# Kernel optimization log

Measured on AMD Instinct MI355X. Metric: run time of the kernel, lower is better.

Reference implementation:

```python
import jax, jax.numpy as jnp
import numpy as np

B, T, D = 4, 2048, 1024
H, KVH = 16, 4          # query heads, kv heads
HD = D // H             # head_dim = 64
R = 32                  # partial rope dims
ROPE_BASE = 10000.0
EPS = 1e-6


def rmsnorm(x, scale):
    # per-head RMSNorm over last dim, computed in fp32 like the torch code
    xf = x.astype(jnp.float32)
    norm = jax.lax.rsqrt(jnp.mean(xf * xf, axis=-1, keepdims=True) + EPS)
    return (xf * norm).astype(x.dtype) * scale


def apply_rope(x, cos, sin):
    # x: (B,T,H,HD); rotate first R dims, pass the rest through
    x_r, x_p = x[..., :R], x[..., R:]
    half = R // 2
    x1, x2 = x_r[..., :half], x_r[..., half:]
    rotated = jnp.concatenate([x1 * cos - x2 * sin, x1 * sin + x2 * cos], axis=-1)
    return jnp.concatenate([rotated, x_p], axis=-1)


def setup_inputs() -> dict:
    key = jax.random.key(0)
    ks = jax.random.split(key, 8)
    x = jax.random.normal(ks[0], (B, T, D), dtype=jnp.float32)
    # RoPE tables exactly as RotaryEmbedding.get_cos_sin
    inv_freq = 1.0 / (ROPE_BASE ** (jnp.arange(0, R, 2, dtype=jnp.float32) / R))
    t = jnp.arange(T, dtype=jnp.float32)
    freqs = jnp.outer(t, inv_freq)                      # (T, R/2)
    cos = jnp.cos(freqs)[None, :, None, :]              # (1,T,1,R/2)
    sin = jnp.sin(freqs)[None, :, None, :]
    s = 1.0 / np.sqrt(D)
    Wq = jax.random.normal(ks[1], (D, D), dtype=jnp.float32) * s
    Wk = jax.random.normal(ks[2], (KVH * HD, D), dtype=jnp.float32) * s
    Wv = jax.random.normal(ks[3], (KVH * HD, D), dtype=jnp.float32) * s
    Wo = jax.random.normal(ks[4], (D, D), dtype=jnp.float32) * s
    q_scale = jnp.ones((HD,), dtype=jnp.float32)
    k_scale = jnp.ones((HD,), dtype=jnp.float32)
    return {"x": x, "cos": cos, "sin": sin, "Wq": Wq, "Wk": Wk, "Wv": Wv,
            "Wo": Wo, "q_scale": q_scale, "k_scale": k_scale}


def reference(x, cos, sin, Wq, Wk, Wv, Wo, q_scale, k_scale):
    b, t, d = x.shape
    q = jnp.einsum('btd,ed->bte', x, Wq).reshape(b, t, H, HD)
    k = jnp.einsum('btd,ed->bte', x, Wk).reshape(b, t, KVH, HD)
    v = jnp.einsum('btd,ed->bte', x, Wv).reshape(b, t, KVH, HD)
    q = apply_rope(rmsnorm(q, q_scale), cos, sin)
    k = apply_rope(rmsnorm(k, k_scale), cos, sin)
    groups = H // KVH
    k = jnp.repeat(k, groups, axis=2)   # (b,t,H,HD), matches repeat_interleave dim=2
    v = jnp.repeat(v, groups, axis=2)
    q = q.transpose(0, 2, 1, 3)         # (b,H,t,HD)
    k = k.transpose(0, 2, 1, 3)
    v = v.transpose(0, 2, 1, 3)
    scores = jnp.einsum('bhqd,bhkd->bhqk', q, k) / np.sqrt(HD)
    causal = jnp.tril(jnp.ones((t, t), dtype=bool))
    scores = jnp.where(causal, scores, -jnp.inf)
    attn = jax.nn.softmax(scores, axis=-1)
    y = jnp.einsum('bhqk,bhkd->bhqd', attn, v)
    y = y.transpose(0, 2, 1, 3).reshape(b, t, d)
    return jnp.einsum('btd,ed->bte', y, Wo)
```

## Files before the change

kernel.cpp:

```cpp
#include <hip/hip_runtime.h>
#include <hip/hip_bf16.h>
#include <stdint.h>

typedef __attribute__((ext_vector_type(8)))  __bf16 bf16x8;
typedef __attribute__((ext_vector_type(4)))  float  f32x4;
typedef __attribute__((ext_vector_type(16))) float  f32x16;
typedef __hip_bfloat16 bf16_t;

#define T_SEQ 2048
#define D_MODEL 1024
#define N_HEADS 16
#define N_KV 4
#define HD 64
#define LDQKV 1536
#define KDIM 1024

__device__ inline void cvt16(const float4* __restrict__ g, int4* __restrict__ s) {
  float4 v0 = g[0], v1 = g[1], v2 = g[2], v3 = g[3];
  union { int4 i[2]; __hip_bfloat162 h[8]; } u;
  u.h[0] = __float22bfloat162_rn(make_float2(v0.x, v0.y));
  u.h[1] = __float22bfloat162_rn(make_float2(v0.z, v0.w));
  u.h[2] = __float22bfloat162_rn(make_float2(v1.x, v1.y));
  u.h[3] = __float22bfloat162_rn(make_float2(v1.z, v1.w));
  u.h[4] = __float22bfloat162_rn(make_float2(v2.x, v2.y));
  u.h[5] = __float22bfloat162_rn(make_float2(v2.z, v2.w));
  u.h[6] = __float22bfloat162_rn(make_float2(v3.x, v3.y));
  u.h[7] = __float22bfloat162_rn(make_float2(v3.z, v3.w));
  s[0] = u.i[0]; s[1] = u.i[1];
}

__device__ inline void storeC(bf16_t* p, float v) { *p = __float2bfloat16(v); }
__device__ inline void storeC(float* p, float v) { *p = v; }

__device__ inline void plswap(unsigned& a, unsigned& b) {
  asm volatile("v_permlane32_swap_b32 %0, %1" : "+v"(a), "+v"(b));
}

__device__ inline float fexp2(float x) {
  float r; asm("v_exp_f32 %0, %1" : "=v"(r) : "v"(x)); return r;
}
__device__ inline unsigned cvtpk(float lo, float hi) {
  unsigned r; asm("v_cvt_pk_bf16_f32 %0, %1, %2" : "=v"(r) : "v"(lo), "v"(hi));
  return r;
}

__device__ inline void gll16(const bf16_t* g, bf16_t* l) {
  __builtin_amdgcn_global_load_lds(
      (const __attribute__((address_space(1))) void*)g,
      (__attribute__((address_space(3))) void*)l, 16, 0, 0);
}

__global__ __launch_bounds__(256) void all_cvt(
    const float* __restrict__ x,
    const float* __restrict__ Wq, const float* __restrict__ Wk,
    const float* __restrict__ Wv, const float* __restrict__ Wo,
    bf16_t* __restrict__ xb, bf16_t* __restrict__ wqkvb,
    bf16_t* __restrict__ wob) {
  const int i = blockIdx.x * 256 + threadIdx.x;
  const float* s; bf16_t* d; int off;
  if (i < 524288)      { s = x;  d = xb;                   off = i; }
  else if (i < 589824) { s = Wq; d = wqkvb;                off = i - 524288; }
  else if (i < 606208) { s = Wk; d = wqkvb + 1024 * 1024;  off = i - 589824; }
  else if (i < 622592) { s = Wv; d = wqkvb + 1280 * 1024;  off = i - 606208; }
  else                 { s = Wo; d = wob;                  off = i - 622592; }
  cvt16((const float4*)s + off * 4, (int4*)d + off * 2);
}

template <int MODE, typename CT>
__global__ __launch_bounds__(256) void gemm_bb(
    const bf16_t* __restrict__ A, const bf16_t* __restrict__ W,
    CT* __restrict__ C, const int ldC,
    const float* __restrict__ cosb, const float* __restrict__ sinb,
    const float* __restrict__ qs, const float* __restrict__ ks,
    bf16_t* __restrict__ v_t)
{
  __shared__ bf16_t As[128 * 32];
  __shared__ bf16_t Bs[128 * 32];
  const int tid = threadIdx.x;
  const int lane = tid & 63;
  const int wv = tid >> 6;
  const int wr = wv >> 1, wc = wv & 1;
  const int m0 = blockIdx.y * 128;
  const int n0 = blockIdx.x * 128;

  const int srow = lane >> 2;
  const int scol = (lane & 3) * 8;
  const bf16_t* gA = A + (size_t)(m0 + 32 * wv + srow) * KDIM + scol;
  const bf16_t* gB = W + (size_t)(n0 + 32 * wv + srow) * KDIM + scol;
  bf16_t* lA = As + wv * 1024;
  bf16_t* lB = Bs + wv * 1024;

  f32x4 acc[4][4];
#pragma unroll
  for (int m = 0; m < 4; ++m)
#pragma unroll
    for (int n = 0; n < 4; ++n)
      acc[m][n] = {0.f, 0.f, 0.f, 0.f};

  const int fr = lane & 15;
  const int fq = lane >> 4;

  for (int k0 = 0; k0 < KDIM; k0 += 32) {
    gll16(gA + k0, lA);
    gll16(gA + 16 * KDIM + k0, lA + 512);
    gll16(gB + k0, lB);
    gll16(gB + 16 * KDIM + k0, lB + 512);
    __syncthreads();
    bf16x8 af[4], bfv[4];
#pragma unroll
    for (int m = 0; m < 4; ++m)
      af[m] = *(const bf16x8*)(&As[(wr * 64 + m * 16 + fr) * 32 + fq * 8]);
#pragma unroll
    for (int n = 0; n < 4; ++n)
      bfv[n] = *(const bf16x8*)(&Bs[(wc * 64 + n * 16 + fr) * 32 + fq * 8]);
#pragma unroll
    for (int m = 0; m < 4; ++m)
#pragma unroll
      for (int n = 0; n < 4; ++n)
        acc[m][n] = __builtin_amdgcn_mfma_f32_16x16x32_bf16(af[m], bfv[n],
                                                            acc[m][n], 0, 0, 0);
    __syncthreads();
  }

  if (MODE == 0 || n0 < 1280) {
    if (MODE == 1) {
      const float* stab = (n0 < 1024) ? qs : ks;
      float sc0 = stab[fr], sc1 = stab[16 + fr], sc2 = stab[32 + fr], sc3 = stab[48 + fr];
#pragma unroll
      for (int m = 0; m < 4; ++m)
#pragma unroll
        for (int r = 0; r < 4; ++r) {
          const int row = m0 + wr * 64 + m * 16 + fq * 4 + r;
          const int t = row & (T_SEQ - 1);
          float ss = acc[m][0][r] * acc[m][0][r] + acc[m][1][r] * acc[m][1][r]
                   + acc[m][2][r] * acc[m][2][r] + acc[m][3][r] * acc[m][3][r];
          ss += __shfl_xor(ss, 1);
          ss += __shfl_xor(ss, 2);
          ss += __shfl_xor(ss, 4);
          ss += __shfl_xor(ss, 8);
          const float nrm = rsqrtf(ss * (1.f / 64.f) + 1e-6f);
          const float v0 = acc[m][0][r] * nrm * sc0;
          const float v1 = acc[m][1][r] * nrm * sc1;
          const float v2 = acc[m][2][r] * nrm * sc2;
          const float v3 = acc[m][3][r] * nrm * sc3;
          const float c = cosb[t * 16 + fr];
          const float s = sinb[t * 16 + fr];
          const float r0 = v0 * c - v1 * s;
          const float r1 = v0 * s + v1 * c;
          bf16_t* p = (bf16_t*)C + (size_t)row * ldC + n0 + wc * 64 + fr;
          p[0]  = __float2bfloat16(r0);
          p[16] = __float2bfloat16(r1);
          p[32] = __float2bfloat16(v2);
          p[48] = __float2bfloat16(v3);
        }
    } else {
#pragma unroll
      for (int m = 0; m < 4; ++m)
#pragma unroll
        for (int n = 0; n < 4; ++n)
#pragma unroll
          for (int r = 0; r < 4; ++r) {
            const int row = wr * 64 + m * 16 + fq * 4 + r;
            const int col = wc * 64 + n * 16 + fr;
            storeC(&C[(size_t)(m0 + row) * ldC + n0 + col], acc[m][n][r]);
          }
    }
  } else {
#pragma unroll
    for (int m = 0; m < 4; ++m) {
      const int row0 = m0 + wr * 64 + m * 16 + fq * 4;
      const int b = row0 >> 11, t0 = row0 & (T_SEQ - 1);
#pragma unroll
      for (int n = 0; n < 4; ++n) {
        const int vcol = n0 - 1280 + wc * 64 + n * 16 + fr;
        const int g = b * 4 + (vcol >> 6);
        const int d = vcol & 63;
        uint2 pk2;
        pk2.x = cvtpk(acc[m][n][0], acc[m][n][1]);
        pk2.y = cvtpk(acc[m][n][2], acc[m][n][3]);
        *(uint2*)(v_t + ((size_t)g * HD + d) * T_SEQ + t0) = pk2;
      }
    }
  }
}

__global__ __launch_bounds__(512) void attn(
    const bf16_t* __restrict__ qkv, const bf16_t* __restrict__ v_t,
    bf16_t* __restrict__ y)
{
  __shared__ int4 lds[2048];
  const int tid  = threadIdx.x;
  const int lane = tid & 63;
  const int w    = tid >> 6;
  const int spair= w >> 1;
  const int h    = w & 1;
  const int ql   = lane & 31;
  const int hi   = lane >> 5;
  const int id   = (int)blockIdx.x;
  const int low3 = id & 7;
  const int rest = id >> 3;
  const int gsel = rest & 1;
  const int hh   = (rest >> 1) & 3;
  const int sbi  = rest >> 3;
  const int sb   = ((sbi >> 2) & 1) ? (sbi + 4 - ((sbi >> 3) << 4)) : (15 - sbi);
  const int g16  = low3 + 8 * gsel;
  const int b    = g16 >> 2, kvh = g16 & 3;
  const int hd   = kvh * 4 + hh;
  const int s    = 4 * sb + spair;
  const int q_glob = s * 32 + ql;
  const int nt   = s + 1;
  const int nR   = 2 * sb + 2;
  const float SCALE_LOG2 = 0.125f * 1.44269504089f;

  const int sid = tid & 255;
  const int u   = tid >> 8;
  const int kr = sid >> 3, kslot = sid & 7;
  const int vd = sid >> 2, vslot = sid & 3;
  const bf16_t* gK = qkv + (size_t)(b * T_SEQ + kr + u * 32) * LDQKV + 1024 + kvh * HD + kslot * 8;
  const bf16_t* gV = v_t + (size_t)((b * N_KV + kvh) * HD + vd) * T_SEQ + vslot * 8 + u * 32;
  const int wKidx = u * 256 + kr * 8 + (kslot ^ (kr & 7));
  const int wVidx = 512 + u * 256 + vd * 4 + (vslot ^ ((vd >> 1) & 3));

  int kridx[4];
#pragma unroll
  for (int c = 0; c < 4; ++c)
    kridx[c] = ql * 8 + ((2 * c + hi) ^ (ql & 7));
  const int vsw = (ql >> 1) & 3;
  const int v0idx = 512 + ql * 4 + (hi ^ vsw);
  const int v1idx = 512 + ql * 4 + ((2 + hi) ^ vsw);
  const int v2idx = 512 + (ql + 32) * 4 + (hi ^ vsw);
  const int v3idx = 512 + (ql + 32) * 4 + ((2 + hi) ^ vsw);

  union ob { unsigned uu[4]; bf16x8 v; } onesf;
#pragma unroll
  for (int i = 0; i < 4; ++i) onesf.uu[i] = 0x3F803F80u;

  f32x16 zro;
#pragma unroll
  for (int i = 0; i < 16; ++i) zro[i] = 0.f;

  float* lf = (float*)lds;

  const bf16_t* Qrow = qkv + (size_t)(b * T_SEQ + q_glob) * LDQKV + hd * HD + hi * 8;
  bf16x8 qfrag[4];
#pragma unroll
  for (int c = 0; c < 4; ++c) {
    bf16x8 raw = *(const bf16x8*)(Qrow + c * 16);
    bf16x8 sc;
#pragma unroll
    for (int j = 0; j < 8; ++j)
      sc[j] = (__bf16)((float)raw[j] * SCALE_LOG2);
    qfrag[c] = sc;
  }

  f32x16 acc0, acc1, accL;
#pragma unroll
  for (int i = 0; i < 16; ++i) { acc0[i] = 0.f; acc1[i] = 0.f; accL[i] = 0.f; }
  float m_run = -1e30f;

  {
    int4 kA = *(const int4*)gK;
    int4 vA = *(const int4*)gV;
    lds[wKidx] = kA;
    lds[wVidx] = vA;
  }
  __syncthreads();

  int buf = 0;
  for (int r = 0; r < nR; ++r) {
    int4 kA, vA;
    const bool more = (r + 1 < nR);
    if (more) {
      kA = *(const int4*)(gK + (size_t)(r + 1) * 64 * LDQKV);
      vA = *(const int4*)(gV + (r + 1) * 64);
    }

    const int t = 2 * r + h;
    if (t < nt) {
      const int k0 = t << 5;
      const bool masked = (t == nt - 1);
      const int base = buf * 1024 + h * 256;

      bf16x8 kf0 = *(const bf16x8*)&lds[base + kridx[0]];
      bf16x8 kf1 = *(const bf16x8*)&lds[base + kridx[1]];
      bf16x8 kf2 = *(const bf16x8*)&lds[base + kridx[2]];
      bf16x8 kf3 = *(const bf16x8*)&lds[base + kridx[3]];

      __builtin_amdgcn_s_setprio(1);
      f32x16 st = __builtin_amdgcn_mfma_f32_32x32x16_bf16(kf0, qfrag[0], zro, 0, 0, 0);
      st = __builtin_amdgcn_mfma_f32_32x32x16_bf16(kf1, qfrag[1], st, 0, 0, 0);
      st = __builtin_amdgcn_mfma_f32_32x32x16_bf16(kf2, qfrag[2], st, 0, 0, 0);
      st = __builtin_amdgcn_mfma_f32_32x32x16_bf16(kf3, qfrag[3], st, 0, 0, 0);
      __builtin_amdgcn_s_setprio(0);

      if (masked) {
#pragma unroll
        for (int rr = 0; rr < 16; ++rr) {
          const int kg = k0 + (rr & 3) + 8 * (rr >> 2) + 4 * hi;
          if (kg > q_glob) st[rr] = -1e30f;
        }
      }
      float m01 = fmaxf(fmaxf(st[0], st[1]), st[2]);
      float m02 = fmaxf(fmaxf(st[3], st[4]), st[5]);
      float m03 = fmaxf(fmaxf(st[6], st[7]), st[8]);
      float m04 = fmaxf(fmaxf(st[9], st[10]), st[11]);
      float m05 = fmaxf(fmaxf(st[12], st[13]), st[14]);
      float m06 = fmaxf(fmaxf(m01, m02), m03);
      float m07 = fmaxf(fmaxf(m04, m05), st[15]);
      const float bmax = fmaxf(m06, m07);
      if (__any(bmax > m_run + 8.f)) {
        const float rmax = fmaxf(bmax, __shfl_xor(bmax, 32));
        const float mnew = fmaxf(m_run, rmax);
        const float corr = fexp2(m_run - mnew);
#pragma unroll
        for (int i = 0; i < 16; ++i) { acc0[i] *= corr; acc1[i] *= corr; }
        accL[0] *= corr;
        m_run = mnew;
      }
      float pp[16];
#pragma unroll
      for (int rr = 0; rr < 16; ++rr) pp[rr] = fexp2(st[rr] - m_run);

      unsigned wp[8];
#pragma unroll
      for (int i = 0; i < 8; ++i) wp[i] = cvtpk(pp[2 * i], pp[2 * i + 1]);
      plswap(wp[0], wp[2]); plswap(wp[1], wp[3]);
      plswap(wp[4], wp[6]); plswap(wp[5], wp[7]);
      union fu { unsigned uu2[4]; bf16x8 v; };
      fu f1, f2;
      f1.uu2[0] = wp[0]; f1.uu2[1] = wp[1]; f1.uu2[2] = wp[2]; f1.uu2[3] = wp[3];
      f2.uu2[0] = wp[4]; f2.uu2[1] = wp[5]; f2.uu2[2] = wp[6]; f2.uu2[3] = wp[7];

      bf16x8 vf0 = *(const bf16x8*)&lds[base + v0idx];
      bf16x8 vf1 = *(const bf16x8*)&lds[base + v1idx];
      bf16x8 vf2 = *(const bf16x8*)&lds[base + v2idx];
      bf16x8 vf3 = *(const bf16x8*)&lds[base + v3idx];

      __builtin_amdgcn_s_setprio(1);
      acc0 = __builtin_amdgcn_mfma_f32_32x32x16_bf16(vf0, f1.v, acc0, 0, 0, 0);
      acc0 = __builtin_amdgcn_mfma_f32_32x32x16_bf16(vf1, f2.v, acc0, 0, 0, 0);
      acc1 = __builtin_amdgcn_mfma_f32_32x32x16_bf16(vf2, f1.v, acc1, 0, 0, 0);
      acc1 = __builtin_amdgcn_mfma_f32_32x32x16_bf16(vf3, f2.v, acc1, 0, 0, 0);
      accL = __builtin_amdgcn_mfma_f32_32x32x16_bf16(onesf.v, f1.v, accL, 0, 0, 0);
      accL = __builtin_amdgcn_mfma_f32_32x32x16_bf16(onesf.v, f2.v, accL, 0, 0, 0);
      __builtin_amdgcn_s_setprio(0);
    }

    if (more) {
      const int nb = (buf ^ 1) * 1024;
      lds[nb + wKidx] = kA;
      lds[nb + wVidx] = vA;
    }
    __syncthreads();
    buf ^= 1;
  }

  float cA = 1.f, cB = 0.f, l_mrg = 0.f;
  if (h == 1) {
    const int fb = spair * 1216 + lane * 19;
#pragma unroll
    for (int i = 0; i < 16; ++i) lf[fb + i] = acc0[i];
    lf[fb + 16] = m_run;
    lf[fb + 17] = accL[0];
  }
  __syncthreads();
  if (h == 0) {
    const int fb = spair * 1216 + lane * 19;
    const float mB = lf[fb + 16], lB = lf[fb + 17];
    const float mM = fmaxf(m_run, mB);
    cA = fexp2(m_run - mM);
    cB = fexp2(mB - mM);
    l_mrg = accL[0] * cA + lB * cB;
#pragma unroll
    for (int i = 0; i < 16; ++i) acc0[i] = acc0[i] * cA + lf[fb + i] * cB;
  }
  __syncthreads();
  if (h == 1) {
    const int fb2 = spair * 1088 + lane * 17;
#pragma unroll
    for (int i = 0; i < 16; ++i) lf[fb2 + i] = acc1[i];
  }
  __syncthreads();
  if (h == 0) {
    const int fb2 = spair * 1088 + lane * 17;
#pragma unroll
    for (int i = 0; i < 16; ++i) acc1[i] = acc1[i] * cA + lf[fb2 + i] * cB;
    const float inv = 1.f / l_mrg;
    bf16_t* yrow = y + (size_t)(b * T_SEQ + q_glob) * D_MODEL + hd * HD;
#pragma unroll
    for (int gg = 0; gg < 4; ++gg) {
      uint2 o0, o1;
      o0.x = cvtpk(acc0[4 * gg + 0] * inv, acc0[4 * gg + 1] * inv);
      o0.y = cvtpk(acc0[4 * gg + 2] * inv, acc0[4 * gg + 3] * inv);
      o1.x = cvtpk(acc1[4 * gg + 0] * inv, acc1[4 * gg + 1] * inv);
      o1.y = cvtpk(acc1[4 * gg + 2] * inv, acc1[4 * gg + 3] * inv);
      *(uint2*)(yrow + 8 * gg + 4 * hi)      = o0;
      *(uint2*)(yrow + 32 + 8 * gg + 4 * hi) = o1;
    }
  }
}

extern "C" void kernel_launch(void* const* d_in, const int* in_sizes, int n_in,
                              void* d_out, int out_size, void* d_ws,
                              size_t ws_size, hipStream_t stream) {
  const float* x    = (const float*)d_in[0];
  const float* cosb = (const float*)d_in[1];
  const float* sinb = (const float*)d_in[2];
  const float* Wq   = (const float*)d_in[3];
  const float* Wk   = (const float*)d_in[4];
  const float* Wv   = (const float*)d_in[5];
  const float* Wo   = (const float*)d_in[6];
  const float* qs   = (const float*)d_in[7];
  const float* ks   = (const float*)d_in[8];
  float* out = (float*)d_out;

  char* ws = (char*)d_ws;
  bf16_t* qkv   = (bf16_t*)ws;
  bf16_t* v_t   = (bf16_t*)(ws + 25165824);
  bf16_t* y     = (bf16_t*)(ws + 29360128);
  bf16_t* xb    = y;
  bf16_t* wqkvb = (bf16_t*)(ws + 46137344);
  bf16_t* wob   = (bf16_t*)(ws + 49283072);

  all_cvt<<<dim3(2688), 256, 0, stream>>>(x, Wq, Wk, Wv, Wo, xb, wqkvb, wob);

  gemm_bb<1, bf16_t><<<dim3(12, 64), 256, 0, stream>>>(
      xb, wqkvb, qkv, LDQKV, cosb, sinb, qs, ks, v_t);
  attn<<<dim3(1024), 512, 0, stream>>>(qkv, v_t, y);
  gemm_bb<0, float><<<dim3(8, 64), 256, 0, stream>>>(
      y, wob, out, D_MODEL, nullptr, nullptr, nullptr, nullptr, nullptr);
}
```

Baseline: 152.9 us.

## Remap GEMM blocks per XCD and stage V transpose through LDS

GEMM launches become a 1D grid whose block index is remapped so that each XCD processes consecutive N tiles of the same M rows, which should improve L2 reuse of the A tiles. The V-transpose epilogue now goes through a swizzled LDS buffer, so v_t is written as contiguous 16-element rows instead of scattered 8-byte stores. The QK epilogue packs bf16 pairs with cvtpk. This adds extra syncthreads and LDS traffic to the V-tile blocks.

```diff
diff --git a/kernel.cpp b/kernel.cpp
--- a/kernel.cpp
+++ b/kernel.cpp
@@ -66,7 +66,7 @@
   cvt16((const float4*)s + off * 4, (int4*)d + off * 2);
 }
 
-template <int MODE, typename CT>
+template <int MODE, int NX, typename CT>
 __global__ __launch_bounds__(256) void gemm_bb(
     const bf16_t* __restrict__ A, const bf16_t* __restrict__ W,
     CT* __restrict__ C, const int ldC,
@@ -74,14 +74,20 @@
     const float* __restrict__ qs, const float* __restrict__ ks,
     bf16_t* __restrict__ v_t)
 {
-  __shared__ bf16_t As[128 * 32];
-  __shared__ bf16_t Bs[128 * 32];
+  __shared__ bf16_t Smem[8192];
+  bf16_t* As = Smem;
+  bf16_t* Bs = Smem + 4096;
   const int tid = threadIdx.x;
   const int lane = tid & 63;
   const int wv = tid >> 6;
   const int wr = wv >> 1, wc = wv & 1;
-  const int m0 = blockIdx.y * 128;
-  const int n0 = blockIdx.x * 128;
+  const int id  = (int)blockIdx.x;
+  const int xcd = id & 7;
+  const int seq = id >> 3;
+  const int mp  = (seq / NX) * 8 + xcd;
+  const int nt  = seq - (seq / NX) * NX;
+  const int m0 = mp * 128;
+  const int n0 = nt * 128;
 
   const int srow = lane >> 2;
   const int scol = (lane & 3) * 8;
@@ -145,13 +151,14 @@
           const float v3 = acc[m][3][r] * nrm * sc3;
           const float c = cosb[t * 16 + fr];
           const float s = sinb[t * 16 + fr];
-          const float r0 = v0 * c - v1 * s;
-          const float r1 = v0 * s + v1 * c;
+          union { unsigned u; bf16_t hh[2]; } pa, pb;
+          pa.u = cvtpk(v0 * c - v1 * s, v0 * s + v1 * c);
+          pb.u = cvtpk(v2, v3);
           bf16_t* p = (bf16_t*)C + (size_t)row * ldC + n0 + wc * 64 + fr;
-          p[0]  = __float2bfloat16(r0);
-          p[16] = __float2bfloat16(r1);
-          p[32] = __float2bfloat16(v2);
-          p[48] = __float2bfloat16(v3);
+          p[0]  = pa.hh[0];
+          p[16] = pa.hh[1];
+          p[32] = pb.hh[0];
+          p[48] = pb.hh[1];
         }
     } else {
 #pragma unroll
@@ -166,20 +173,45 @@
           }
     }
   } else {
-#pragma unroll
-    for (int m = 0; m < 4; ++m) {
-      const int row0 = m0 + wr * 64 + m * 16 + fq * 4;
-      const int b = row0 >> 11, t0 = row0 & (T_SEQ - 1);
-#pragma unroll
-      for (int n = 0; n < 4; ++n) {
-        const int vcol = n0 - 1280 + wc * 64 + n * 16 + fr;
-        const int g = b * 4 + (vcol >> 6);
-        const int d = vcol & 63;
-        uint2 pk2;
-        pk2.x = cvtpk(acc[m][n][0], acc[m][n][1]);
-        pk2.y = cvtpk(acc[m][n][2], acc[m][n][3]);
-        *(uint2*)(v_t + ((size_t)g * HD + d) * T_SEQ + t0) = pk2;
+    const int b4 = (m0 >> 11) * 4;
+    const int t0base = m0 & (T_SEQ - 1);
+    const int vcol = tid & 127;
+    const int vc = n0 - 1280 + vcol;
+    const int g = b4 + (vc >> 6);
+    const int d = vc & 63;
+#pragma unroll
+    for (int half = 0; half < 2; ++half) {
+      if (wr == half) {
+#pragma unroll
+        for (int m = 0; m < 4; ++m)
+#pragma unroll
+          for (int n = 0; n < 4; ++n)
+#pragma unroll
+            for (int r2 = 0; r2 < 4; r2 += 2) {
+              union { unsigned u; bf16_t hh[2]; } pk2;
+              pk2.u = cvtpk(acc[m][n][r2], acc[m][n][r2 + 1]);
+              const int tl0 = m * 16 + fq * 4 + r2;
+              const int col = wc * 64 + n * 16 + fr;
+              const int sw = ((tl0 >> 2) & 7) << 4;
+              Smem[tl0 * 128 + (col ^ sw)]       = pk2.hh[0];
+              Smem[(tl0 + 1) * 128 + (col ^ sw)] = pk2.hh[1];
+            }
       }
+      __syncthreads();
+      bf16_t* dst0 = v_t + ((size_t)(g * HD + d)) * T_SEQ + t0base + half * 64;
+#pragma unroll
+      for (int ci = 0; ci < 2; ++ci) {
+        const int cu = (tid >> 7) + ci * 2;
+        union { int4 q[2]; bf16_t hh[16]; } ld;
+#pragma unroll
+        for (int t = 0; t < 16; ++t) {
+          const int tt = cu * 16 + t;
+          ld.hh[t] = Smem[tt * 128 + (vcol ^ (((tt >> 2) & 7) << 4))];
+        }
+        *(int4*)(dst0 + cu * 16)     = ld.q[0];
+        *(int4*)(dst0 + cu * 16 + 8) = ld.q[1];
+      }
+      __syncthreads();
     }
   }
 }
@@ -424,9 +456,9 @@
 
   all_cvt<<<dim3(2688), 256, 0, stream>>>(x, Wq, Wk, Wv, Wo, xb, wqkvb, wob);
 
-  gemm_bb<1, bf16_t><<<dim3(12, 64), 256, 0, stream>>>(
+  gemm_bb<1, 12, bf16_t><<<dim3(768), 256, 0, stream>>>(
       xb, wqkvb, qkv, LDQKV, cosb, sinb, qs, ks, v_t);
   attn<<<dim3(1024), 512, 0, stream>>>(qkv, v_t, y);
-  gemm_bb<0, float><<<dim3(8, 64), 256, 0, stream>>>(
+  gemm_bb<0, 8, float><<<dim3(512), 256, 0, stream>>>(
       y, wob, out, D_MODEL, nullptr, nullptr, nullptr, nullptr, nullptr);
 }
```

New measurement: 149.3 us. 1.02x faster.

## Split RMSNorm/RoPE and V transpose out of GEMM epilogue; XCD-aware block mapping

Applied to the files above, without the earlier changes.

The QKV GEMM no longer applies RMSNorm, RoPE and the V transpose in its epilogue. Those steps now run in two new kernels: a per-row rms_rope pass over the bf16 qkv buffer and a tiled LDS transpose that writes v_t. Both GEMMs also switch to a 1D grid that remaps block ids so that blocks on the same XCD share M tiles, aiming for better L2 reuse. The cost is two extra launches and an extra read and write pass over qkv, traded for a simpler epilogue and coalesced V stores.

```diff
diff --git a/kernel.cpp b/kernel.cpp
--- a/kernel.cpp
+++ b/kernel.cpp
@@ -66,13 +66,10 @@
   cvt16((const float4*)s + off * 4, (int4*)d + off * 2);
 }
 
-template <int MODE, typename CT>
+template <int NX, typename CT>
 __global__ __launch_bounds__(256) void gemm_bb(
     const bf16_t* __restrict__ A, const bf16_t* __restrict__ W,
-    CT* __restrict__ C, const int ldC,
-    const float* __restrict__ cosb, const float* __restrict__ sinb,
-    const float* __restrict__ qs, const float* __restrict__ ks,
-    bf16_t* __restrict__ v_t)
+    CT* __restrict__ C, const int ldC)
 {
   __shared__ bf16_t As[128 * 32];
   __shared__ bf16_t Bs[128 * 32];
@@ -80,8 +77,13 @@
   const int lane = tid & 63;
   const int wv = tid >> 6;
   const int wr = wv >> 1, wc = wv & 1;
-  const int m0 = blockIdx.y * 128;
-  const int n0 = blockIdx.x * 128;
+  const int id  = (int)blockIdx.x;
+  const int xcd = id & 7;
+  const int seq = id >> 3;
+  const int mp  = (seq / NX) * 8 + xcd;
+  const int nt  = seq - (seq / NX) * NX;
+  const int m0 = mp * 128;
+  const int n0 = nt * 128;
 
   const int srow = lane >> 2;
   const int scol = (lane & 3) * 8;
@@ -122,66 +124,68 @@
     __syncthreads();
   }
 
-  if (MODE == 0 || n0 < 1280) {
-    if (MODE == 1) {
-      const float* stab = (n0 < 1024) ? qs : ks;
-      float sc0 = stab[fr], sc1 = stab[16 + fr], sc2 = stab[32 + fr], sc3 = stab[48 + fr];
-#pragma unroll
-      for (int m = 0; m < 4; ++m)
-#pragma unroll
-        for (int r = 0; r < 4; ++r) {
-          const int row = m0 + wr * 64 + m * 16 + fq * 4 + r;
-          const int t = row & (T_SEQ - 1);
-          float ss = acc[m][0][r] * acc[m][0][r] + acc[m][1][r] * acc[m][1][r]
-                   + acc[m][2][r] * acc[m][2][r] + acc[m][3][r] * acc[m][3][r];
-          ss += __shfl_xor(ss, 1);
-          ss += __shfl_xor(ss, 2);
-          ss += __shfl_xor(ss, 4);
-          ss += __shfl_xor(ss, 8);
-          const float nrm = rsqrtf(ss * (1.f / 64.f) + 1e-6f);
-          const float v0 = acc[m][0][r] * nrm * sc0;
-          const float v1 = acc[m][1][r] * nrm * sc1;
-          const float v2 = acc[m][2][r] * nrm * sc2;
-          const float v3 = acc[m][3][r] * nrm * sc3;
-          const float c = cosb[t * 16 + fr];
-          const float s = sinb[t * 16 + fr];
-          const float r0 = v0 * c - v1 * s;
-          const float r1 = v0 * s + v1 * c;
-          bf16_t* p = (bf16_t*)C + (size_t)row * ldC + n0 + wc * 64 + fr;
-          p[0]  = __float2bfloat16(r0);
-          p[16] = __float2bfloat16(r1);
-          p[32] = __float2bfloat16(v2);
-          p[48] = __float2bfloat16(v3);
-        }
-    } else {
-#pragma unroll
-      for (int m = 0; m < 4; ++m)
-#pragma unroll
-        for (int n = 0; n < 4; ++n)
-#pragma unroll
-          for (int r = 0; r < 4; ++r) {
-            const int row = wr * 64 + m * 16 + fq * 4 + r;
-            const int col = wc * 64 + n * 16 + fr;
-            storeC(&C[(size_t)(m0 + row) * ldC + n0 + col], acc[m][n][r]);
-          }
-    }
-  } else {
-#pragma unroll
-    for (int m = 0; m < 4; ++m) {
-      const int row0 = m0 + wr * 64 + m * 16 + fq * 4;
-      const int b = row0 >> 11, t0 = row0 & (T_SEQ - 1);
-#pragma unroll
-      for (int n = 0; n < 4; ++n) {
-        const int vcol = n0 - 1280 + wc * 64 + n * 16 + fr;
-        const int g = b * 4 + (vcol >> 6);
-        const int d = vcol & 63;
-        uint2 pk2;
-        pk2.x = cvtpk(acc[m][n][0], acc[m][n][1]);
-        pk2.y = cvtpk(acc[m][n][2], acc[m][n][3]);
-        *(uint2*)(v_t + ((size_t)g * HD + d) * T_SEQ + t0) = pk2;
+#pragma unroll
+  for (int m = 0; m < 4; ++m)
+#pragma unroll
+    for (int n = 0; n < 4; ++n)
+#pragma unroll
+      for (int r = 0; r < 4; ++r) {
+        const int row = wr * 64 + m * 16 + fq * 4 + r;
+        const int col = wc * 64 + n * 16 + fr;
+        storeC(&C[(size_t)(m0 + row) * ldC + n0 + col], acc[m][n][r]);
       }
-    }
-  }
+}
+
+__global__ __launch_bounds__(256) void rms_rope(
+    bf16_t* __restrict__ qkv, const float* __restrict__ cosb,
+    const float* __restrict__ sinb, const float* __restrict__ qs,
+    const float* __restrict__ ks)
+{
+  const int row = blockIdx.x;
+  const int t = row & (T_SEQ - 1);
+  const int tid = threadIdx.x;
+  const int lane = tid & 63;
+  const int wv = tid >> 6;
+  const int f = lane & 15;
+  const float c = (lane < 32) ? cosb[t * 16 + f] : 0.f;
+  const float s = (lane < 32) ? sinb[t * 16 + f] : 0.f;
+  for (int hh = wv; hh < 20; hh += 4) {
+    const size_t idx = (size_t)row * LDQKV + hh * 64 + lane;
+    const float v = __bfloat162float(qkv[idx]);
+    float ssum = v * v;
+#pragma unroll
+    for (int off = 32; off; off >>= 1) ssum += __shfl_xor(ssum, off);
+    const float norm = rsqrtf(ssum * (1.f / 64.f) + 1e-6f);
+    const float scale = (hh < 16 ? qs : ks)[lane];
+    float val = v * norm * scale;
+    const float partner = __shfl_xor(val, 16);
+    if (lane < 16)      val = val * c - partner * s;
+    else if (lane < 32) val = partner * s + val * c;
+    qkv[idx] = __float2bfloat16(val);
+  }
+}
+
+__global__ __launch_bounds__(256) void v_transpose(
+    const bf16_t* __restrict__ qkv, bf16_t* __restrict__ v_t)
+{
+  __shared__ bf16_t tile[64 * 72];
+  const int g = blockIdx.x;
+  const int t0 = blockIdx.y * 64;
+  const int tid = threadIdx.x;
+  const int i = tid >> 2;
+  const int dc = (tid & 3) * 16;
+  const bf16_t* src = qkv + (size_t)((g >> 2) * T_SEQ + t0 + i) * LDQKV
+                      + 1280 + (g & 3) * HD + dc;
+  const int4* gs = (const int4*)src;
+  int4 x0 = gs[0], x1 = gs[1];
+  int4* st = (int4*)(&tile[i * 72 + dc]);
+  st[0] = x0; st[1] = x1;
+  __syncthreads();
+  union { int4 v[2]; bf16_t h[16]; } u;
+#pragma unroll
+  for (int j = 0; j < 16; ++j) u.h[j] = tile[(dc + j) * 72 + i];
+  int4* dst = (int4*)(v_t + (size_t)(g * HD + i) * T_SEQ + t0 + dc);
+  dst[0] = u.v[0]; dst[1] = u.v[1];
 }
 
 __global__ __launch_bounds__(512) void attn(
@@ -424,9 +428,9 @@
 
   all_cvt<<<dim3(2688), 256, 0, stream>>>(x, Wq, Wk, Wv, Wo, xb, wqkvb, wob);
 
-  gemm_bb<1, bf16_t><<<dim3(12, 64), 256, 0, stream>>>(
-      xb, wqkvb, qkv, LDQKV, cosb, sinb, qs, ks, v_t);
+  gemm_bb<12, bf16_t><<<dim3(768), 256, 0, stream>>>(xb, wqkvb, qkv, LDQKV);
+  rms_rope<<<dim3(8192), 256, 0, stream>>>(qkv, cosb, sinb, qs, ks);
+  v_transpose<<<dim3(16, 32), 256, 0, stream>>>(qkv, v_t);
   attn<<<dim3(1024), 512, 0, stream>>>(qkv, v_t, y);
-  gemm_bb<0, float><<<dim3(8, 64), 256, 0, stream>>>(
-      y, wob, out, D_MODEL, nullptr, nullptr, nullptr, nullptr, nullptr);
-}
+  gemm_bb<8, float><<<dim3(512), 256, 0, stream>>>(y, wob, out, D_MODEL);
+}
```

Measured after the change: 154.9 us. Within noise of the previous version (+1.3%).
